# Kernel tuning notes

Measured on AMD Instinct MI355X. Metric: run time of the kernel, lower is better.

## Reference

```python
import jax, jax.numpy as jnp
import numpy as np

N, T, OBS, ACT, H = 4096, 256, 32, 8, 64
FORGET_BIAS = 1.0


def setup_inputs() -> dict:
    key = jax.random.key(0)
    k1, k2, k3, k4, k5 = jax.random.split(key, 5)
    return {
        "obss": jax.random.normal(k1, (N, T, OBS), dtype=jnp.float32),
        "actions": jax.random.normal(k2, (N, T, ACT), dtype=jnp.float32),
        "W_lstm": jax.random.normal(k3, (OBS + ACT + H, 4 * H), dtype=jnp.float32) * 0.1,
        "b_lstm": jnp.zeros((4 * H,), dtype=jnp.float32),
        "W_dec": jax.random.normal(k4, (H, 1), dtype=jnp.float32),
        "b_dec": jax.random.normal(k5, (1,), dtype=jnp.float32),
    }


def reference(obss, actions, W_lstm, b_lstm, W_dec, b_dec):
    # concat obs+action features: [N, T, OBS+ACT] -> time-major [T, N, D]
    x = jnp.concatenate([obss, actions], axis=-1)
    x = jnp.transpose(x, (1, 0, 2))
    n = x.shape[1]
    c0 = jnp.zeros((n, H), dtype=x.dtype)
    h0 = jnp.zeros((n, H), dtype=x.dtype)

    def step(carry, xt):
        c, h = carry
        # TF BasicLSTMCell: gates ordered i, j (candidate), f, o
        gates = jnp.concatenate([xt, h], axis=1) @ W_lstm + b_lstm
        i, j, f, o = jnp.split(gates, 4, axis=1)
        new_c = c * jax.nn.sigmoid(f + FORGET_BIAS) + jax.nn.sigmoid(i) * jnp.tanh(j)
        new_h = jnp.tanh(new_c) * jax.nn.sigmoid(o)
        return (new_c, new_h), new_h

    _, hs = jax.lax.scan(step, (c0, h0), x)  # hs: [T, N, H]
    # per-timestep linear decode: [T, N, 1]
    out = hs @ W_dec + b_dec
    return out
```

## Files before the change

### kernel.cpp

```cpp
#include <hip/hip_runtime.h>
#include <cstddef>

#define T_STEPS 256
#define OBS     32
#define ACTD    8
#define NB      16
#define HPAD    88
#define NSEQ    4096

typedef _Float16 f16x8 __attribute__((ext_vector_type(8)));
typedef _Float16 f16x4 __attribute__((ext_vector_type(4)));
typedef _Float16 f16x2 __attribute__((ext_vector_type(2)));
typedef float    f32x4 __attribute__((ext_vector_type(4)));

union F8 { f16x8 v; _Float16 e[8]; f16x2 h2[4]; };
union F4 { f16x4 v; _Float16 e[4]; f16x2 h2[2]; };

#define LOG2E 1.44269504088896f

__device__ __forceinline__ float fsig(float x) {
    return __builtin_amdgcn_rcpf(1.0f + __builtin_amdgcn_exp2f(x * -LOG2E));
}
__device__ __forceinline__ f16x2 pkrtz(float a, float b) {
    return __builtin_bit_cast(f16x2, __builtin_amdgcn_cvt_pkrtz(a, b));
}

__global__ __launch_bounds__(512)
void lstm_fused(const float* __restrict__ obss, const float* __restrict__ actions,
                const float* __restrict__ W, const float* __restrict__ b,
                const float* __restrict__ Wdec, const float* __restrict__ bdec_p,
                float* __restrict__ out)
{
    __shared__ __align__(16) _Float16 Ah[2][NB * HPAD];
    __shared__ __align__(16) float partb[2][16][20];
    __shared__ __align__(16) float pbuf[2][4][4][4][16][4];

    const int tid  = threadIdx.x;
    const int w8   = tid >> 6;
    const int w    = w8 & 3;
    const bool isA = w8 < 4;
    const int lane = tid & 63;
    const int g    = lane >> 4;
    const int m    = lane & 15;
    const int n0   = blockIdx.x * NB;
    const int u0   = 16 * w + 4 * g;
    const int sigb = 32 * (w >> 1) + 8 * g + 4 * (w & 1);

    f16x8 Ahh[4][2];
    f16x8 Axo[4], AxA[4];
    f32x4 wdv = {0.f, 0.f, 0.f, 0.f};
    {
        const float* Wc = W + 16 * w + m;
        if (isA) {
#pragma unroll
            for (int e = 0; e < 4; e++) {
#pragma unroll
                for (int c = 0; c < 2; c++) {
                    F8 hi;
#pragma unroll
                    for (int i = 0; i < 8; i++) {
                        int k = 32 * c + 16 * (i >> 2) + 4 * g + (i & 3);
                        hi.e[i] = (_Float16)Wc[(40 + k) * 256 + 64 * e];
                    }
                    Ahh[e][c] = hi.v;
                }
            }
            wdv = *(const f32x4*)&Wdec[u0];
        } else {
#pragma unroll
            for (int e = 0; e < 4; e++) {
                F8 xo, xA;
                float bv = b[64 * e + 16 * w + m] + (e == 2 ? 1.0f : 0.0f);
#pragma unroll
                for (int i = 0; i < 8; i++) {
                    int d = 16 * (i >> 2) + 4 * g + (i & 3);
                    xo.e[i] = (_Float16)Wc[d * 256 + 64 * e];
                    xA.e[i] = (d < ACTD) ? (_Float16)Wc[(OBS + d) * 256 + 64 * e]
                            : (d == 8)   ? (_Float16)bv
                                         : (_Float16)0.0f;
                }
                Axo[e] = xo.v;
                AxA[e] = xA.v;
            }
        }
    }
    const float bd = bdec_p[0];

    for (int i = tid; i < 2 * NB * HPAD; i += 512)
        (&Ah[0][0])[i] = (_Float16)0.0f;

    const float* pO = obss    + ((size_t)(n0 + m) * T_STEPS) * OBS  + 4 * g;
    const float* pA = actions + ((size_t)(n0 + m) * T_STEPS) * ACTD + 4 * g;
    f32x4 xo0 = {0,0,0,0}, xo1 = {0,0,0,0}, xa = {0,0,0,0};
    auto loadx = [&]() {
        xo0 = *(const f32x4*)pO;
        xo1 = *(const f32x4*)(pO + 16);
        pO += OBS;
        if (g < 2) { xa = *(const f32x4*)pA; pA += ACTD; }
    };
    f16x8 bxo, bxA;
    auto cvtx = [&]() {
        F8 uo;
        uo.h2[0] = pkrtz(xo0[0], xo0[1]);
        uo.h2[1] = pkrtz(xo0[2], xo0[3]);
        uo.h2[2] = pkrtz(xo1[0], xo1[1]);
        uo.h2[3] = pkrtz(xo1[2], xo1[3]);
        F8 uA;
        uA.h2[0] = pkrtz(g == 2 ? 1.0f : xa[0], xa[1]);
        uA.h2[1] = pkrtz(xa[2], xa[3]);
        uA.h2[2] = pkrtz(0.0f, 0.0f);
        uA.h2[3] = pkrtz(0.0f, 0.0f);
        bxo = uo.v;
        bxA = uA.v;
    };
    auto pmm_store = [&](int buf) {
        const f32x4 z = {0.f, 0.f, 0.f, 0.f};
#pragma unroll
        for (int e = 0; e < 4; e++) {
            f32x4 pc = __builtin_amdgcn_mfma_f32_16x16x32_f16(Axo[e], bxo, z, 0, 0, 0);
            pc = __builtin_amdgcn_mfma_f32_16x16x32_f16(AxA[e], bxA, pc, 0, 0, 0);
            *(f32x4*)&pbuf[buf][w][e][g][m][0] = pc;
        }
    };

    if (!isA) {
        loadx();
        cvtx();
        pmm_store(0);
        loadx();
    }
    f32x4 cr = {0.f, 0.f, 0.f, 0.f};
    float* pOut = out + (size_t)((w + 3) & 3) * NSEQ + n0 + lane;

    __syncthreads();
    if (isA) __builtin_amdgcn_s_setprio(1);

#pragma unroll 2
    for (int t = 0; t < T_STEPS; ++t) {
        const int cb  = t & 1;
        const int nb2 = cb ^ 1;
        asm volatile("s_waitcnt lgkmcnt(0)\n\ts_barrier" ::: "memory");

        if (isA) {
            const _Float16* bh = &Ah[cb][m * HPAD];
            f16x8 bh0 = *(const f16x8*)(bh + 8 * g);
            f16x8 bh1 = *(const f16x8*)(bh + 32 + 8 * g);

            f32x4 acc[4];
#pragma unroll
            for (int e = 0; e < 4; e++) {
                f32x4 pe = *(const f32x4*)&pbuf[cb][w][e][g][m][0];
                f32x4 a = __builtin_amdgcn_mfma_f32_16x16x32_f16(Ahh[e][0], bh0, pe, 0, 0, 0);
                a = __builtin_amdgcn_mfma_f32_16x16x32_f16(Ahh[e][1], bh1, a, 0, 0, 0);
                acc[e] = a;
            }

            float h4[4];
#pragma unroll
            for (int r = 0; r < 4; r++) {
                float sf = fsig(acc[2][r]);
                float ei = __builtin_amdgcn_exp2f(acc[0][r] * -LOG2E);
                float ej = __builtin_amdgcn_exp2f(acc[1][r] * (-2.0f * LOG2E));
                float A = 1.0f + ei, B = 1.0f + ej;
                float prod = (B - 2.0f) * __builtin_amdgcn_rcpf(A * B);
                float c = cr[r] * sf + prod;
                cr[r] = c;
                float ec = __builtin_amdgcn_exp2f(c * (-2.0f * LOG2E));
                float eo = __builtin_amdgcn_exp2f(acc[3][r] * -LOG2E);
                float D = 1.0f + ec, E = 1.0f + eo;
                h4[r] = (D - 2.0f) * __builtin_amdgcn_rcpf(D * E);
            }
            F4 hi_;
            hi_.h2[0] = pkrtz(h4[0], h4[1]);
            hi_.h2[1] = pkrtz(h4[2], h4[3]);
            *(f16x4*)(&Ah[nb2][m * HPAD + sigb]) = hi_.v;

            float p = h4[0] * wdv[0];
            p = fmaf(h4[1], wdv[1], p);
            p = fmaf(h4[2], wdv[2], p);
            p = fmaf(h4[3], wdv[3], p);
            partb[cb][m][4 * w + g] = p;
        } else {
            if (t + 1 < T_STEPS) {
                cvtx();
                pmm_store(nb2);
            }
            if (t + 2 < T_STEPS) loadx();

            if (t > 0 && w == (t & 3) && lane < 16) {
                const float* pp = &partb[nb2][lane][0];
                f32x4 q0 = *(const f32x4*)pp;
                f32x4 q1 = *(const f32x4*)(pp + 4);
                f32x4 q2 = *(const f32x4*)(pp + 8);
                f32x4 q3 = *(const f32x4*)(pp + 12);
                f32x4 s4 = (q0 + q1) + (q2 + q3);
                *pOut = s4[0] + s4[1] + s4[2] + s4[3] + bd;
                pOut += 4 * NSEQ;
            }
        }
    }
    if (isA) __builtin_amdgcn_s_setprio(0);

    __syncthreads();
    if (!isA && w == 0 && lane < 16) {
        const float* pp = &partb[1][lane][0];
        f32x4 q0 = *(const f32x4*)pp;
        f32x4 q1 = *(const f32x4*)(pp + 4);
        f32x4 q2 = *(const f32x4*)(pp + 8);
        f32x4 q3 = *(const f32x4*)(pp + 12);
        f32x4 s4 = (q0 + q1) + (q2 + q3);
        *pOut = s4[0] + s4[1] + s4[2] + s4[3] + bd;
    }
}

extern "C" void kernel_launch(void* const* d_in, const int* in_sizes, int n_in,
                              void* d_out, int out_size, void* d_ws, size_t ws_size,
                              hipStream_t stream) {
    (void)in_sizes; (void)n_in; (void)d_ws; (void)ws_size; (void)out_size;
    const float* obss    = (const float*)d_in[0];
    const float* actions = (const float*)d_in[1];
    const float* W       = (const float*)d_in[2];
    const float* b       = (const float*)d_in[3];
    const float* Wdec    = (const float*)d_in[4];
    const float* bdec    = (const float*)d_in[5];
    float* out = (float*)d_out;
    lstm_fused<<<dim3(NSEQ / NB), dim3(512), 0, stream>>>(obss, actions, W, b, Wdec, bdec, out);
}
```

Measured before the change: 145.7 us.

## Move input projection MFMAs into recurrent waves via shared fp16 operand staging

Helper waves no longer compute the x@W input-gate projection with MFMA and store fp32 partials. Instead they stage the fp16 inputs (plus a constant-1 bias column) into an extended shared operand buffer next to h, and the recurrent waves run four MFMAs per gate split into two independent accumulation chains. The gate math also folds the forget sigmoid into one reciprocal. This removes the fp32 partial store and reload, but adds MFMA work to the critical recurrent path.

```diff
diff --git a/kernel.cpp b/kernel.cpp
--- a/kernel.cpp
+++ b/kernel.cpp
@@ -5,7 +5,7 @@
 #define OBS     32
 #define ACTD    8
 #define NB      16
-#define HPAD    88
+#define HPAD2   152
 #define NSEQ    4096
 
 typedef _Float16 f16x8 __attribute__((ext_vector_type(8)));
@@ -18,9 +18,6 @@
 
 #define LOG2E 1.44269504088896f
 
-__device__ __forceinline__ float fsig(float x) {
-    return __builtin_amdgcn_rcpf(1.0f + __builtin_amdgcn_exp2f(x * -LOG2E));
-}
 __device__ __forceinline__ f16x2 pkrtz(float a, float b) {
     return __builtin_bit_cast(f16x2, __builtin_amdgcn_cvt_pkrtz(a, b));
 }
@@ -31,9 +28,8 @@
                 const float* __restrict__ Wdec, const float* __restrict__ bdec_p,
                 float* __restrict__ out)
 {
-    __shared__ __align__(16) _Float16 Ah[2][NB * HPAD];
+    __shared__ __align__(16) _Float16 Bop[2][NB * HPAD2];
     __shared__ __align__(16) float partb[2][16][20];
-    __shared__ __align__(16) float pbuf[2][4][4][4][16][4];
 
     const int tid  = threadIdx.x;
     const int w8   = tid >> 6;
@@ -46,48 +42,44 @@
     const int u0   = 16 * w + 4 * g;
     const int sigb = 32 * (w >> 1) + 8 * g + 4 * (w & 1);
 
-    f16x8 Ahh[4][2];
-    f16x8 Axo[4], AxA[4];
+    f16x8 AW[4][4];
     f32x4 wdv = {0.f, 0.f, 0.f, 0.f};
-    {
+    if (isA) {
         const float* Wc = W + 16 * w + m;
-        if (isA) {
-#pragma unroll
-            for (int e = 0; e < 4; e++) {
-#pragma unroll
-                for (int c = 0; c < 2; c++) {
-                    F8 hi;
-#pragma unroll
-                    for (int i = 0; i < 8; i++) {
-                        int k = 32 * c + 16 * (i >> 2) + 4 * g + (i & 3);
-                        hi.e[i] = (_Float16)Wc[(40 + k) * 256 + 64 * e];
-                    }
-                    Ahh[e][c] = hi.v;
+#pragma unroll
+        for (int e = 0; e < 4; e++) {
+#pragma unroll
+            for (int c = 0; c < 2; c++) {
+                F8 hi;
+#pragma unroll
+                for (int i = 0; i < 8; i++) {
+                    int k = 32 * c + 16 * (i >> 2) + 4 * g + (i & 3);
+                    hi.e[i] = (_Float16)Wc[(40 + k) * 256 + 64 * e];
                 }
-            }
-            wdv = *(const f32x4*)&Wdec[u0];
-        } else {
-#pragma unroll
-            for (int e = 0; e < 4; e++) {
-                F8 xo, xA;
-                float bv = b[64 * e + 16 * w + m] + (e == 2 ? 1.0f : 0.0f);
-#pragma unroll
-                for (int i = 0; i < 8; i++) {
-                    int d = 16 * (i >> 2) + 4 * g + (i & 3);
-                    xo.e[i] = (_Float16)Wc[d * 256 + 64 * e];
-                    xA.e[i] = (d < ACTD) ? (_Float16)Wc[(OBS + d) * 256 + 64 * e]
-                            : (d == 8)   ? (_Float16)bv
-                                         : (_Float16)0.0f;
-                }
-                Axo[e] = xo.v;
-                AxA[e] = xA.v;
-            }
+                AW[e][c] = hi.v;
+            }
+            F8 xo, xA;
+            float bv = b[64 * e + 16 * w + m] + (e == 2 ? 1.0f : 0.0f);
+#pragma unroll
+            for (int i = 0; i < 8; i++) {
+                int kk = 16 * (i >> 2) + 4 * g + (i & 3);
+                xo.e[i] = (_Float16)Wc[kk * 256 + 64 * e];
+                xA.e[i] = (kk < ACTD) ? (_Float16)Wc[(OBS + kk) * 256 + 64 * e]
+                        : (kk == 16)  ? (_Float16)bv
+                                      : (_Float16)0.0f;
+            }
+            AW[e][2] = xo.v;
+            AW[e][3] = xA.v;
         }
+        wdv = *(const f32x4*)&Wdec[u0];
     }
     const float bd = bdec_p[0];
 
-    for (int i = tid; i < 2 * NB * HPAD; i += 512)
-        (&Ah[0][0])[i] = (_Float16)0.0f;
+    for (int i = tid; i < 2 * NB * HPAD2; i += 512)
+        (&Bop[0][0])[i] = (_Float16)0.0f;
+    __syncthreads();
+    if (tid < 32)
+        Bop[tid >> 4][(tid & 15) * HPAD2 + 100] = (_Float16)1.0f;
 
     const float* pO = obss    + ((size_t)(n0 + m) * T_STEPS) * OBS  + 4 * g;
     const float* pA = actions + ((size_t)(n0 + m) * T_STEPS) * ACTD + 4 * g;
@@ -98,35 +90,30 @@
         pO += OBS;
         if (g < 2) { xa = *(const f32x4*)pA; pA += ACTD; }
     };
-    f16x8 bxo, bxA;
+    f16x8 bxo;
+    f16x4 uaq;
     auto cvtx = [&]() {
         F8 uo;
         uo.h2[0] = pkrtz(xo0[0], xo0[1]);
         uo.h2[1] = pkrtz(xo0[2], xo0[3]);
         uo.h2[2] = pkrtz(xo1[0], xo1[1]);
         uo.h2[3] = pkrtz(xo1[2], xo1[3]);
-        F8 uA;
-        uA.h2[0] = pkrtz(g == 2 ? 1.0f : xa[0], xa[1]);
-        uA.h2[1] = pkrtz(xa[2], xa[3]);
-        uA.h2[2] = pkrtz(0.0f, 0.0f);
-        uA.h2[3] = pkrtz(0.0f, 0.0f);
+        F4 ua_;
+        ua_.h2[0] = pkrtz(xa[0], xa[1]);
+        ua_.h2[1] = pkrtz(xa[2], xa[3]);
         bxo = uo.v;
-        bxA = uA.v;
+        uaq = ua_.v;
     };
-    auto pmm_store = [&](int buf) {
-        const f32x4 z = {0.f, 0.f, 0.f, 0.f};
-#pragma unroll
-        for (int e = 0; e < 4; e++) {
-            f32x4 pc = __builtin_amdgcn_mfma_f32_16x16x32_f16(Axo[e], bxo, z, 0, 0, 0);
-            pc = __builtin_amdgcn_mfma_f32_16x16x32_f16(AxA[e], bxA, pc, 0, 0, 0);
-            *(f32x4*)&pbuf[buf][w][e][g][m][0] = pc;
-        }
+    auto stagex = [&](int buf) {
+        _Float16* xp = &Bop[buf][m * HPAD2 + 64];
+        *(f16x8*)(xp + 8 * g) = bxo;
+        if (g < 2) *(f16x4*)(xp + 32 + 8 * g) = uaq;
     };
 
     if (!isA) {
         loadx();
         cvtx();
-        pmm_store(0);
+        stagex(0);
         loadx();
     }
     f32x4 cr = {0.f, 0.f, 0.f, 0.f};
@@ -142,38 +129,43 @@
         asm volatile("s_waitcnt lgkmcnt(0)\n\ts_barrier" ::: "memory");
 
         if (isA) {
-            const _Float16* bh = &Ah[cb][m * HPAD];
-            f16x8 bh0 = *(const f16x8*)(bh + 8 * g);
-            f16x8 bh1 = *(const f16x8*)(bh + 32 + 8 * g);
+            const _Float16* bp = &Bop[cb][m * HPAD2];
+            f16x8 f0 = *(const f16x8*)(bp + 8 * g);
+            f16x8 f1 = *(const f16x8*)(bp + 32 + 8 * g);
+            f16x8 f2 = *(const f16x8*)(bp + 64 + 8 * g);
+            f16x8 f3 = *(const f16x8*)(bp + 96 + 8 * g);
 
             f32x4 acc[4];
 #pragma unroll
             for (int e = 0; e < 4; e++) {
-                f32x4 pe = *(const f32x4*)&pbuf[cb][w][e][g][m][0];
-                f32x4 a = __builtin_amdgcn_mfma_f32_16x16x32_f16(Ahh[e][0], bh0, pe, 0, 0, 0);
-                a = __builtin_amdgcn_mfma_f32_16x16x32_f16(Ahh[e][1], bh1, a, 0, 0, 0);
-                acc[e] = a;
+                const f32x4 z = {0.f, 0.f, 0.f, 0.f};
+                f32x4 aA = __builtin_amdgcn_mfma_f32_16x16x32_f16(AW[e][2], f2, z, 0, 0, 0);
+                f32x4 aB = __builtin_amdgcn_mfma_f32_16x16x32_f16(AW[e][3], f3, z, 0, 0, 0);
+                aA = __builtin_amdgcn_mfma_f32_16x16x32_f16(AW[e][0], f0, aA, 0, 0, 0);
+                aB = __builtin_amdgcn_mfma_f32_16x16x32_f16(AW[e][1], f1, aB, 0, 0, 0);
+                acc[e] = aA + aB;
             }
 
             float h4[4];
 #pragma unroll
             for (int r = 0; r < 4; r++) {
-                float sf = fsig(acc[2][r]);
+                float ef = __builtin_amdgcn_exp2f(acc[2][r] * -LOG2E);
                 float ei = __builtin_amdgcn_exp2f(acc[0][r] * -LOG2E);
                 float ej = __builtin_amdgcn_exp2f(acc[1][r] * (-2.0f * LOG2E));
-                float A = 1.0f + ei, B = 1.0f + ej;
-                float prod = (B - 2.0f) * __builtin_amdgcn_rcpf(A * B);
-                float c = cr[r] * sf + prod;
+                float Fv = 1.0f + ef, Av = 1.0f + ei, Bv = 1.0f + ej;
+                float AB = Av * Bv;
+                float num = fmaf(cr[r], AB, Fv * (Bv - 2.0f));
+                float c = num * __builtin_amdgcn_rcpf(Fv * AB);
                 cr[r] = c;
                 float ec = __builtin_amdgcn_exp2f(c * (-2.0f * LOG2E));
                 float eo = __builtin_amdgcn_exp2f(acc[3][r] * -LOG2E);
-                float D = 1.0f + ec, E = 1.0f + eo;
-                h4[r] = (D - 2.0f) * __builtin_amdgcn_rcpf(D * E);
+                float Dv = 1.0f + ec, Ev = 1.0f + eo;
+                h4[r] = (Dv - 2.0f) * __builtin_amdgcn_rcpf(Dv * Ev);
             }
             F4 hi_;
             hi_.h2[0] = pkrtz(h4[0], h4[1]);
             hi_.h2[1] = pkrtz(h4[2], h4[3]);
-            *(f16x4*)(&Ah[nb2][m * HPAD + sigb]) = hi_.v;
+            *(f16x4*)(&Bop[nb2][m * HPAD2 + sigb]) = hi_.v;
 
             float p = h4[0] * wdv[0];
             p = fmaf(h4[1], wdv[1], p);
@@ -183,7 +175,7 @@
         } else {
             if (t + 1 < T_STEPS) {
                 cvtx();
-                pmm_store(nb2);
+                stagex(nb2);
             }
             if (t + 2 < T_STEPS) loadx();
 
```

Result: faster. 133.8 us (-8.2%).
